# Kernel tuning notes

Hardware: AMD Instinct MI355X
Metric: run time of the kernel (lower is better)

Reference implementation:

```python
import jax, jax.numpy as jnp
import numpy as np

F_DIM = 128; K_RBF = 64; NBLOCKS = 3; NUM_SCC = 1; IBEGIN = 4
N_RES_INT = 2; N_RES_AT = 2; N_RES_OUT = 1
NUM_OUTPUTS = 2001; NOUTS = NUM_OUTPUTS + 4  # +4 charge-equilibration channels when num_scc>0
N_ATOMS = 10000; DEG = 32; N_EDGES = N_ATOMS * DEG; NMOL = 64
CUTOFF = 10.0
LOG2 = 0.6931471805599453


def ssp(x):
    # shifted softplus
    return jax.nn.softplus(x) - LOG2


def _residual(x, W1, b1, W2, b2):
    y = ssp(x) @ W1 + b1
    return x + ssp(y) @ W2 + b2


def _forward(R, M, QaAlpha, QaBeta,
             em_W0, em_b0, em_W1, em_b1, em_W2, em_b2,
             iWrbf, iWi, ibi, iWj, ibj, irW1, irb1, irW2, irb2, iWout, ibout, iu,
             arW1, arb1, arW2, arb2, orW1, orb1, orW2, orb2, oW,
             Z, idx_i, idx_j, mol_idx):
    N = R.shape[0]
    dt = R.dtype
    # --- interatomic distances via neighbor gather ---
    Dvec = R[idx_i] - R[idx_j]                                # [E,3]
    Dij = jnp.sqrt(jax.nn.relu(jnp.sum(Dvec * Dvec, -1)))     # [E]
    # --- PhysNet-style exp-Gaussian RBF expansion with smooth cutoff ---
    mu = jnp.linspace(np.exp(-CUTOFF), 1.0, K_RBF).astype(dt)
    gamma = jnp.asarray((K_RBF / (2.0 * (1.0 - np.exp(-CUTOFF)))) ** 2, dt)
    t = Dij / CUTOFF
    cut = jnp.where(Dij < CUTOFF, 1.0 - 6.0 * t**5 + 15.0 * t**4 - 10.0 * t**3, 0.0)
    rbf = cut[:, None] * jnp.exp(-gamma * (jnp.exp(-Dij)[:, None] - mu) ** 2)  # [E,K]

    seg_mol = lambda v: jax.ops.segment_sum(v, mol_idx, num_segments=NMOL)
    Zf = Z.astype(dt)[:, None]
    QaA, QaB = QaAlpha, QaBeta
    QAlpha_mol = seg_mol(QaA)
    QBeta_mol = seg_mol(QaB)
    outputs = None
    nhloss = jnp.asarray(0.0, dt)
    for j in range(NUM_SCC + 1):
        # elemental-modes embedding: f = [Z, M, QaAlpha, QaBeta] -> F
        f = jnp.concatenate([Zf, M[:, None], QaA[:, None], QaB[:, None]], 1)  # [N,4]
        h = ssp(f @ em_W0 + em_b0)
        h = ssp(h @ em_W1 + em_b1)
        x = h @ em_W2 + em_b2                                 # [N,F]
        outputs = jnp.zeros((N, NOUTS), dt)
        nhloss = jnp.asarray(0.0, dt)
        lastout2 = None
        for i in range(NBLOCKS):
            # --- interaction (message passing: gather -> multiply -> segment_sum) ---
            xa = ssp(x)
            g = rbf @ iWrbf[i]                                # [E,F]
            xi = ssp(xa @ iWi[i] + ibi[i])                    # [N,F]
            xj = ssp(xa @ iWj[i] + ibj[i])                    # [N,F]
            m = xi + jax.ops.segment_sum(g * xj[idx_j], idx_i, num_segments=N)
            for r in range(N_RES_INT):
                m = _residual(m, irW1[i, r], irb1[i, r], irW2[i, r], irb2[i, r])
            m = ssp(m)
            x = iu[i] * x + m @ iWout[i] + ibout[i]           # gated update
            for r in range(N_RES_AT):
                x = _residual(x, arW1[i, r], arb1[i, r], arW2[i, r], arb2[i, r])
            # --- output block ---
            xo = x
            for r in range(N_RES_OUT):
                xo = _residual(xo, orW1[i, r], orb1[i, r], orW2[i, r], orb2[i, r])
            out = ssp(xo) @ oW[i]                             # [N,NOUTS]
            outputs = outputs + out
            if j == NUM_SCC:
                out2 = out[IBEGIN:] ** 2                      # row slice, as in source
                if i > 0:
                    nhloss = nhloss + jnp.mean(out2 / (out2 + lastout2 + 1e-7))
                lastout2 = out2
        # --- NSE charge equilibration (per-molecule segment sums) ---
        QaA_n, faA = outputs[:, 0], outputs[:, 1]
        QaB_n, faB = outputs[:, 2], outputs[:, 3]
        QaA = QaA_n + faA * ((QAlpha_mol - seg_mol(QaA_n)) / seg_mol(faA))[mol_idx]
        QaB = QaB_n + faB * ((QBeta_mol - seg_mol(QaB_n)) / seg_mol(faB))[mol_idx]
    outputs = outputs[:, IBEGIN:]
    outputs = jnp.concatenate([outputs[:, :1], jax.nn.relu(outputs[:, 1:])], 1)
    return outputs, Dij, nhloss


def setup_inputs() -> dict:
    key = jax.random.key(0)
    ks = iter(jax.random.split(key, 64))
    nrm = lambda shp, scale: jax.random.normal(next(ks), shp, jnp.float32) * scale
    F, K, B = F_DIM, K_RBF, NBLOCKS
    s = F ** -0.5
    inp = {}
    inp["R"] = jax.random.uniform(next(ks), (N_ATOMS, 3), jnp.float32, 0.0, 12.0)
    inp["M"] = jax.random.uniform(next(ks), (N_ATOMS,), jnp.float32, 1.0, 32.0)
    inp["QaAlpha"] = nrm((N_ATOMS,), 0.1)
    inp["QaBeta"] = nrm((N_ATOMS,), 0.1)
    # elemental-modes MLP 4 -> F -> F -> F
    inp["em_W0"] = nrm((4, F), 0.5); inp["em_b0"] = nrm((F,), 0.01)
    inp["em_W1"] = nrm((F, F), s);   inp["em_b1"] = nrm((F,), 0.01)
    inp["em_W2"] = nrm((F, F), s);   inp["em_b2"] = nrm((F,), 0.01)
    # interaction blocks (stacked over NBLOCKS)
    inp["iWrbf"] = nrm((B, K, F), K ** -0.5)
    inp["iWi"] = nrm((B, F, F), s); inp["ibi"] = nrm((B, F), 0.01)
    inp["iWj"] = nrm((B, F, F), s); inp["ibj"] = nrm((B, F), 0.01)
    inp["irW1"] = nrm((B, N_RES_INT, F, F), s); inp["irb1"] = nrm((B, N_RES_INT, F), 0.01)
    inp["irW2"] = nrm((B, N_RES_INT, F, F), s); inp["irb2"] = nrm((B, N_RES_INT, F), 0.01)
    inp["iWout"] = nrm((B, F, F), s); inp["ibout"] = nrm((B, F), 0.01)
    inp["iu"] = jnp.ones((B, F), jnp.float32)
    inp["arW1"] = nrm((B, N_RES_AT, F, F), s); inp["arb1"] = nrm((B, N_RES_AT, F), 0.01)
    inp["arW2"] = nrm((B, N_RES_AT, F, F), s); inp["arb2"] = nrm((B, N_RES_AT, F), 0.01)
    inp["orW1"] = nrm((B, N_RES_OUT, F, F), s); inp["orb1"] = nrm((B, N_RES_OUT, F), 0.01)
    inp["orW2"] = nrm((B, N_RES_OUT, F, F), s); inp["orb2"] = nrm((B, N_RES_OUT, F), 0.01)
    inp["oW"] = nrm((B, F, NOUTS), s)
    # integer graph structure
    inp["Z"] = jax.random.randint(next(ks), (N_ATOMS,), 1, 36, jnp.int32)
    idx_i = jnp.repeat(jnp.arange(N_ATOMS, dtype=jnp.int32), DEG)
    rnd = jax.random.randint(next(ks), (N_EDGES,), 1, N_ATOMS, jnp.int32)
    inp["idx_i"] = idx_i
    inp["idx_j"] = (idx_i + rnd) % N_ATOMS  # never self -> Dij > 0
    inp["mol_idx"] = ((jnp.arange(N_ATOMS) * NMOL) // N_ATOMS).astype(jnp.int32)
    return inp


def reference(R, M, QaAlpha, QaBeta,
              em_W0, em_b0, em_W1, em_b1, em_W2, em_b2,
              iWrbf, iWi, ibi, iWj, ibj, irW1, irb1, irW2, irb2, iWout, ibout, iu,
              arW1, arb1, arW2, arb2, orW1, orb1, orW2, orb2, oW,
              Z, idx_i, idx_j, mol_idx):
    return _forward(R, M, QaAlpha, QaBeta,
                    em_W0, em_b0, em_W1, em_b1, em_W2, em_b2,
                    iWrbf, iWi, ibi, iWj, ibj, irW1, irb1, irW2, irb2, iWout, ibout, iu,
                    arW1, arb1, arW2, arb2, orW1, orb1, orW2, orb2, oW,
                    Z, idx_i, idx_j, mol_idx)
```

## Files before the change

### kernel.cpp

```cpp
#include <hip/hip_runtime.h>
#include <math.h>

#define NA 10000
#define NAP 10048
#define FD 128
#define KR 64
#define DEGC 32
#define NE (NA*DEGC)
#define NOUTS_C 2005
#define NOUT_FINAL 2001

typedef __attribute__((ext_vector_type(8))) short bh8;
typedef __attribute__((ext_vector_type(4))) float fx4;

__device__ __forceinline__ float sspf(float x){
    float ex = __expf(-fabsf(x));
    return fmaxf(x, 0.0f) + __logf(1.0f + ex) - 0.6931471805599453f;
}
__device__ __forceinline__ unsigned short f2bf(float x){
    unsigned int u = __float_as_uint(x);
    unsigned int r = (u + 0x7fffu + ((u >> 16) & 1u)) >> 16;
    return (unsigned short)r;
}
__device__ __forceinline__ float bf2f(unsigned short u){
    return __uint_as_float(((unsigned int)u) << 16);
}
__device__ __forceinline__ fx4 mfma16(bh8 a, bh8 b, fx4 c){
    return __builtin_amdgcn_mfma_f32_16x16x32_bf16(a, b, c, 0, 0, 0);
}
__device__ __forceinline__ void gll16(const void* g, void* l){
    __builtin_amdgcn_global_load_lds(
        (const __attribute__((address_space(1))) unsigned int*)g,
        (__attribute__((address_space(3))) unsigned int*)l, 16, 0, 0);
}

__global__ void k_dij(const float* __restrict__ R, const int* __restrict__ idx_i,
                      const int* __restrict__ idx_j, float* __restrict__ dij_out){
    int e = blockIdx.x*256 + threadIdx.x;
    if (e >= NE) return;
    int i = idx_i[e], j = idx_j[e];
    float dx = R[i*3+0] - R[j*3+0];
    float dy = R[i*3+1] - R[j*3+1];
    float dz = R[i*3+2] - R[j*3+2];
    dij_out[e] = sqrtf(fmaxf(dx*dx + dy*dy + dz*dz, 0.0f));
}

__global__ void k_init(const float* __restrict__ QaAin, const float* __restrict__ QaBin,
                       const int* __restrict__ mol, float* __restrict__ QaA,
                       float* __restrict__ QaB, float* __restrict__ QAmol,
                       float* __restrict__ QBmol){
    int a = blockIdx.x*256 + threadIdx.x;
    if (a >= NA) return;
    float qa = QaAin[a], qb = QaBin[a];
    QaA[a] = qa; QaB[a] = qb;
    int m = mol[a];
    atomicAdd(&QAmol[m], qa);
    atomicAdd(&QBmol[m], qb);
}

__global__ void k_cvtW(const float* __restrict__ em_W1, const float* __restrict__ em_W2,
                       const float* __restrict__ iWi, const float* __restrict__ iWj,
                       const float* __restrict__ iWout, const float* __restrict__ irW1,
                       const float* __restrict__ irW2, const float* __restrict__ arW1,
                       const float* __restrict__ arW2, const float* __restrict__ orW1,
                       const float* __restrict__ orW2, short* __restrict__ img){
    int gid = blockIdx.x*256 + threadIdx.x;
    if (gid >= 41*2048) return;
    int m = gid >> 11;
    int f = gid & 2047;
    int l15 = f & 15, t = f >> 4;
    int g = t & 3, u = t >> 2;
    int kk = u & 3, cg = u >> 2;
    const float* src; int mm;
    if      (m < 1){ src = em_W1; mm = m; }
    else if (m < 2){ src = em_W2; mm = m-1; }
    else if (m < 5){ src = iWi;   mm = m-2; }
    else if (m < 8){ src = iWj;   mm = m-5; }
    else if (m < 11){ src = iWout; mm = m-8; }
    else if (m < 17){ src = irW1;  mm = m-11; }
    else if (m < 23){ src = irW2;  mm = m-17; }
    else if (m < 29){ src = arW1;  mm = m-23; }
    else if (m < 35){ src = arW2;  mm = m-29; }
    else if (m < 38){ src = orW1;  mm = m-35; }
    else            { src = orW2;  mm = m-38; }
    src += (size_t)mm * 16384;
    int n = cg*16 + l15;
    int k0 = (kk*4 + g)*8;
    bh8 pk;
    #pragma unroll
    for (int j = 0; j < 8; ++j) pk[j] = (short)f2bf(src[(k0+j)*128 + n]);
    *(bh8*)&img[m*16384 + f*8] = pk;
}

__global__ void k_cvtB(const float* __restrict__ em_b1, const float* __restrict__ em_b2,
                       const float* __restrict__ ibi, const float* __restrict__ ibj,
                       const float* __restrict__ ibout, const float* __restrict__ irb1,
                       const float* __restrict__ irb2, const float* __restrict__ arb1,
                       const float* __restrict__ arb2, const float* __restrict__ orb1,
                       const float* __restrict__ orb2, const float* __restrict__ iu,
                       float* __restrict__ bimg){
    int gid = blockIdx.x*256 + threadIdx.x;
    if (gid >= 44*128) return;
    int m = gid >> 7, c = gid & 127;
    float v;
    if      (m < 1)  v = em_b1[c];
    else if (m < 2)  v = em_b2[c];
    else if (m < 5)  v = ibi[(m-2)*128+c];
    else if (m < 8)  v = ibj[(m-5)*128+c];
    else if (m < 11) v = ibout[(m-8)*128+c];
    else if (m < 17) v = irb1[(m-11)*128+c];
    else if (m < 23) v = irb2[(m-17)*128+c];
    else if (m < 29) v = arb1[(m-23)*128+c];
    else if (m < 35) v = arb2[(m-29)*128+c];
    else if (m < 38) v = orb1[(m-35)*128+c];
    else if (m < 41) v = orb2[(m-38)*128+c];
    else             v = iu[(m-41)*128+c];
    bimg[gid] = v;
}

__global__ void k_cvt_wrbf(const float* __restrict__ iWrbf, short* __restrict__ img){
    int gid = blockIdx.x*256 + threadIdx.x;
    if (gid >= 3*1024) return;
    int i = gid >> 10;
    int loc = gid & 1023;
    int n = loc >> 3, s = loc & 7;
    const float* src = iWrbf + (size_t)i*8192;
    int kbase = (s ^ (n&7)) * 8;
    bh8 pk;
    #pragma unroll
    for (int j = 0; j < 8; ++j) pk[j] = (short)f2bf(src[(kbase+j)*128 + n]);
    *(bh8*)&img[i*8192 + n*64 + s*8] = pk;
}

__global__ void k_cvt_oW(const float* __restrict__ oW, short* __restrict__ img){
    int gid = blockIdx.x*256 + threadIdx.x;
    if (gid >= 98304) return;
    int l15 = gid & 15;
    int g = (gid >> 4) & 3;
    int nt = (gid >> 6) & 7;
    int rest = gid >> 9;
    int kk2 = rest % 12, cg = rest / 12;
    int seg = kk2 >> 2;
    int n = cg*128 + nt*16 + l15;
    int kbase = (kk2 & 3)*32 + g*8;
    bh8 pk;
    #pragma unroll
    for (int j = 0; j < 8; ++j){
        float v = (n < NOUTS_C) ? oW[((size_t)seg*128 + kbase + j)*NOUTS_C + n] : 0.0f;
        pk[j] = (short)f2bf(v);
    }
    *(bh8*)&img[(size_t)gid*8] = pk;
}

__device__ __forceinline__ void loadB8(const short* __restrict__ W, int g, int l15, int wv, bh8 b[8]){
    const bh8* Wf = (const bh8*)W;
    const int cgA = wv*2, cgB = wv*2 + 1;
    #pragma unroll
    for (int kk = 0; kk < 4; ++kk){
        b[kk]   = Wf[((cgA*4+kk)*4+g)*16 + l15];
        b[4+kk] = Wf[((cgB*4+kk)*4+g)*16 + l15];
    }
}
__device__ __forceinline__ void gemmB(const short* As, const bh8 b[8], int g, int l15, fx4 acc[2]){
    #pragma unroll
    for (int kk = 0; kk < 4; ++kk){
        int q = kk*4 + g;
        bh8 a = *(const bh8*)&As[l15*128 + ((q ^ (l15&7))*8)];
        acc[0] = mfma16(a, b[kk],   acc[0]);
        acc[1] = mfma16(a, b[4+kk], acc[1]);
    }
}
#define ZACC2 { acc[0]=(fx4){0,0,0,0}; acc[1]=(fx4){0,0,0,0}; }

__device__ __forceinline__ void epiS_ts(short* dst, fx4 acc[2], const float* b,
                                        int g, int c0, int c1){
    float b0 = b[c0], b1 = b[c1];
    #pragma unroll
    for (int r = 0; r < 4; ++r){
        int row = g*4 + r;
        dst[row*128 + (((c0>>3) ^ (row&7))*8) + (c0&7)] = (short)f2bf(sspf(acc[0][r] + b0));
        dst[row*128 + (((c1>>3) ^ (row&7))*8) + (c1&7)] = (short)f2bf(sspf(acc[1][r] + b1));
    }
}
__device__ __forceinline__ void epiS_xadd(float xr[2][4], fx4 acc[2], const float* b,
                                          int c0, int c1){
    float b0 = b[c0], b1 = b[c1];
    #pragma unroll
    for (int r = 0; r < 4; ++r){
        xr[0][r] += acc[0][r] + b0;
        xr[1][r] += acc[1][r] + b1;
    }
}
__device__ __forceinline__ void writeS_xr(short* dst, float xr[2][4], int g, int c0, int c1){
    #pragma unroll
    for (int r = 0; r < 4; ++r){
        int row = g*4 + r;
        dst[row*128 + (((c0>>3) ^ (row&7))*8) + (c0&7)] = (short)f2bf(sspf(xr[0][r]));
        dst[row*128 + (((c1>>3) ^ (row&7))*8) + (c1&7)] = (short)f2bf(sspf(xr[1][r]));
    }
}
__device__ __forceinline__ void storeS_xr(float* dst, float xr[2][4], int r0, int g, int c0, int c1){
    #pragma unroll
    for (int r = 0; r < 4; ++r){
        int row = r0 + g*4 + r;
        dst[(size_t)row*FD + c0] = xr[0][r];
        dst[(size_t)row*FD + c1] = xr[1][r];
    }
}
__device__ __forceinline__ void storeS_ssp(float* dst, fx4 acc[2], const float* b,
                                           int r0, int g, int c0, int c1){
    float b0 = b[c0], b1 = b[c1];
    #pragma unroll
    for (int r = 0; r < 4; ++r){
        int row = r0 + g*4 + r;
        dst[(size_t)row*FD + c0] = sspf(acc[0][r] + b0);
        dst[(size_t)row*FD + c1] = sspf(acc[1][r] + b1);
    }
}
__device__ __forceinline__ void stage_A16(short* As, const float* src, int r0, int tid){
    int row = tid >> 4, cb = tid & 15;
    const float* p = src + (size_t)(r0+row)*FD + cb*8;
    float4 u = *(const float4*)p, v = *(const float4*)(p+4);
    float vv[8] = {u.x,u.y,u.z,u.w,v.x,v.y,v.z,v.w};
    bh8 pk;
    #pragma unroll
    for (int t = 0; t < 8; ++t) pk[t] = (short)f2bf(sspf(vv[t]));
    *(bh8*)&As[row*128 + ((cb ^ (row&7))*8)] = pk;
}

__global__ __launch_bounds__(256) void k_pre(
    const short* __restrict__ wimg, const float* __restrict__ bimg,
    const int* __restrict__ Z, const float* __restrict__ M,
    const float* __restrict__ QaA, const float* __restrict__ QaB,
    const float* __restrict__ em_W0, const float* __restrict__ em_b0,
    float* __restrict__ x, float* __restrict__ xi, float* __restrict__ xj)
{
    __shared__ __align__(16) short As[2048];
    __shared__ __align__(16) short Ts[2048];
    __shared__ float fs[16][4];
    const int tid = threadIdx.x, wv = tid>>6, ln = tid&63, g = ln>>4, l15 = ln&15;
    const int r0 = blockIdx.x*16;
    const int c0 = wv*32 + l15, c1 = c0 + 16;
    bh8 bU[8], bV[8];
    if (tid < 64){
        int rr = tid>>2, k = tid&3;
        int a = r0 + rr;
        fs[rr][k] = (k==0) ? (float)Z[a] : (k==1) ? M[a] : (k==2) ? QaA[a] : QaB[a];
    }
    __syncthreads();
    {
        int row = tid>>4, cb = tid&15;
        bh8 pk;
        #pragma unroll
        for (int t = 0; t < 8; ++t){
            int c = cb*8 + t;
            float v = sspf(em_b0[c] + fs[row][0]*em_W0[c] + fs[row][1]*em_W0[128+c]
                           + fs[row][2]*em_W0[256+c] + fs[row][3]*em_W0[384+c]);
            pk[t] = (short)f2bf(v);
        }
        *(bh8*)&As[row*128 + ((cb ^ (row&7))*8)] = pk;
    }
    loadB8(wimg + 0*16384, g, l15, wv, bU);
    __syncthreads();
    fx4 acc[2];
    float xr[2][4];
    ZACC2; gemmB(As, bU, g, l15, acc);
    loadB8(wimg + 1*16384, g, l15, wv, bV);
    epiS_ts(Ts, acc, bimg + 0*128, g, c0, c1);
    __syncthreads();
    ZACC2; gemmB(Ts, bV, g, l15, acc);
    loadB8(wimg + 2*16384, g, l15, wv, bU);
    {
        const float* b = bimg + 1*128;
        float b0 = b[c0], b1 = b[c1];
        #pragma unroll
        for (int r = 0; r < 4; ++r){
            xr[0][r] = acc[0][r] + b0;
            xr[1][r] = acc[1][r] + b1;
        }
    }
    storeS_xr(x, xr, r0, g, c0, c1);
    writeS_xr(As, xr, g, c0, c1);
    __syncthreads();
    ZACC2; gemmB(As, bU, g, l15, acc);
    loadB8(wimg + 5*16384, g, l15, wv, bV);
    storeS_ssp(xi, acc, bimg + 2*128, r0, g, c0, c1);
    ZACC2; gemmB(As, bV, g, l15, acc);
    storeS_ssp(xj, acc, bimg + 5*128, r0, g, c0, c1);
}

__global__ __launch_bounds__(256) void k_post(
    const short* __restrict__ wimg, const float* __restrict__ bimg,
    const float* __restrict__ mb, float* __restrict__ x,
    short* __restrict__ Aimg, float* __restrict__ xi, float* __restrict__ xj,
    int i, int dodual)
{
    __shared__ __align__(16) short As[2048];
    __shared__ __align__(16) short Ts[2048];
    const int tid = threadIdx.x, wv = tid>>6, ln = tid&63, g = ln>>4, l15 = ln&15;
    const int r0 = blockIdx.x*16;
    const int c0 = wv*32 + l15, c1 = c0 + 16;
    bh8 bU[8], bV[8];
    float xr[2][4];
    #pragma unroll
    for (int r = 0; r < 4; ++r){
        size_t row = (size_t)(r0 + g*4 + r);
        xr[0][r] = mb[row*FD + c0];
        xr[1][r] = mb[row*FD + c1];
    }
    stage_A16(As, mb, r0, tid);
    loadB8(wimg + (size_t)(11+2*i)*16384, g, l15, wv, bU);
    __syncthreads();
    fx4 acc[2];
    ZACC2; gemmB(As, bU, g, l15, acc);
    loadB8(wimg + (size_t)(17+2*i)*16384, g, l15, wv, bV);
    epiS_ts(Ts, acc, bimg + (11+2*i)*128, g, c0, c1);
    __syncthreads();
    ZACC2; gemmB(Ts, bV, g, l15, acc);
    loadB8(wimg + (size_t)(12+2*i)*16384, g, l15, wv, bU);
    epiS_xadd(xr, acc, bimg + (17+2*i)*128, c0, c1);
    writeS_xr(As, xr, g, c0, c1);
    __syncthreads();
    ZACC2; gemmB(As, bU, g, l15, acc);
    loadB8(wimg + (size_t)(18+2*i)*16384, g, l15, wv, bV);
    epiS_ts(Ts, acc, bimg + (12+2*i)*128, g, c0, c1);
    __syncthreads();
    ZACC2; gemmB(Ts, bV, g, l15, acc);
    loadB8(wimg + (size_t)(8+i)*16384, g, l15, wv, bU);
    epiS_xadd(xr, acc, bimg + (18+2*i)*128, c0, c1);
    writeS_xr(As, xr, g, c0, c1);
    __syncthreads();
    ZACC2; gemmB(As, bU, g, l15, acc);
    loadB8(wimg + (size_t)(23+2*i)*16384, g, l15, wv, bV);
    {
        const float* bb = bimg + (8+i)*128;
        const float* uu = bimg + (41+i)*128;
        float b0 = bb[c0], b1 = bb[c1], u0 = uu[c0], u1 = uu[c1];
        #pragma unroll
        for (int r = 0; r < 4; ++r){
            size_t row = (size_t)(r0 + g*4 + r);
            xr[0][r] = u0*x[row*FD + c0] + acc[0][r] + b0;
            xr[1][r] = u1*x[row*FD + c1] + acc[1][r] + b1;
        }
    }
    writeS_xr(Ts, xr, g, c0, c1);
    __syncthreads();
    ZACC2; gemmB(Ts, bV, g, l15, acc);
    loadB8(wimg + (size_t)(29+2*i)*16384, g, l15, wv, bU);
    epiS_ts(As, acc, bimg + (23+2*i)*128, g, c0, c1);
    __syncthreads();
    ZACC2; gemmB(As, bU, g, l15, acc);
    loadB8(wimg + (size_t)(24+2*i)*16384, g, l15, wv, bV);
    epiS_xadd(xr, acc, bimg + (29+2*i)*128, c0, c1);
    writeS_xr(Ts, xr, g, c0, c1);
    __syncthreads();
    ZACC2; gemmB(Ts, bV, g, l15, acc);
    loadB8(wimg + (size_t)(30+2*i)*16384, g, l15, wv, bU);
    epiS_ts(As, acc, bimg + (24+2*i)*128, g, c0, c1);
    __syncthreads();
    ZACC2; gemmB(As, bU, g, l15, acc);
    loadB8(wimg + (size_t)(dodual ? (3+i) : (35+i))*16384, g, l15, wv, bV);
    epiS_xadd(xr, acc, bimg + (30+2*i)*128, c0, c1);
    storeS_xr(x, xr, r0, g, c0, c1);
    writeS_xr(Ts, xr, g, c0, c1);
    __syncthreads();
    if (dodual){
        ZACC2; gemmB(Ts, bV, g, l15, acc);
        loadB8(wimg + (size_t)(6+i)*16384, g, l15, wv, bU);
        storeS_ssp(xi, acc, bimg + (3+i)*128, r0, g, c0, c1);
        ZACC2; gemmB(Ts, bU, g, l15, acc);
        loadB8(wimg + (size_t)(35+i)*16384, g, l15, wv, bV);
        storeS_ssp(xj, acc, bimg + (6+i)*128, r0, g, c0, c1);
        ZACC2; gemmB(Ts, bV, g, l15, acc);
        loadB8(wimg + (size_t)(38+i)*16384, g, l15, wv, bU);
        epiS_ts(As, acc, bimg + (35+i)*128, g, c0, c1);
    } else {
        ZACC2; gemmB(Ts, bV, g, l15, acc);
        loadB8(wimg + (size_t)(38+i)*16384, g, l15, wv, bU);
        epiS_ts(As, acc, bimg + (35+i)*128, g, c0, c1);
    }
    __syncthreads();
    ZACC2; gemmB(As, bU, g, l15, acc);
    {
        const float* bb = bimg + (38+i)*128;
        float b0 = bb[c0], b1 = bb[c1];
        #pragma unroll
        for (int r = 0; r < 4; ++r){
            int row = r0 + g*4 + r;
            float v0 = xr[0][r] + acc[0][r] + b0;
            float v1 = xr[1][r] + acc[1][r] + b1;
            int k0 = i*128 + c0, k1 = i*128 + c1;
            Aimg[(size_t)row*384 + (((k0>>3) ^ (row&7))*8) + (k0&7)] = (short)f2bf(sspf(v0));
            Aimg[(size_t)row*384 + (((k1>>3) ^ (row&7))*8) + (k1&7)] = (short)f2bf(sspf(v1));
        }
    }
}

__global__ __launch_bounds__(256) void k_agg_mfma(
    const float* __restrict__ dij, const short* __restrict__ wri,
    const int* __restrict__ idxj, const float* __restrict__ xi,
    const float* __restrict__ xj, float* __restrict__ mout,
    float gamma, float mu0, float dmu)
{
    __shared__ short Rb[256*64];
    __shared__ short Wr[128*64];
    __shared__ int Jd[256];
    const int tid = threadIdx.x;
    const int wv = tid >> 6, ln = tid & 63;
    const int e0 = blockIdx.x * 256;
    {
        const char* g2 = (const char*)wri;
        char* l2 = (char*)Wr;
        #pragma unroll
        for (int i = 0; i < 4; ++i){
            int off = wv*4096 + i*1024;
            gll16(g2 + off + ln*16, l2 + off);
        }
        Jd[tid] = idxj[e0 + tid];
    }
    {
        float d = dij[e0 + tid];
        float t = d * 0.1f;
        float cut = 0.0f;
        if (d < 10.0f){
            float t2 = t*t, t3 = t2*t, t4 = t2*t2, t5 = t4*t;
            cut = 1.0f - 6.0f*t5 + 15.0f*t4 - 10.0f*t3;
        }
        float ed = __expf(-d);
        int row = tid;
        #pragma unroll
        for (int s = 0; s < 8; ++s){
            bh8 pk;
            #pragma unroll
            for (int jj = 0; jj < 8; ++jj){
                float u = ed - (mu0 + (float)(s*8+jj)*dmu);
                pk[jj] = (short)f2bf(cut * __expf(-gamma*u*u));
            }
            *(bh8*)&Rb[row*64 + ((s ^ (row&7))*8)] = pk;
        }
    }
    __syncthreads();
    const int g = ln >> 4, l15 = ln & 15;
    bh8 a[4][2];
    #pragma unroll
    for (int mt = 0; mt < 4; ++mt){
        int el = wv*64 + mt*16 + l15;
        #pragma unroll
        for (int kk = 0; kk < 2; ++kk)
            a[mt][kk] = *(const bh8*)&Rb[el*64 + (((kk*4+g) ^ (el&7))*8)];
    }
    float pa[2][8];
    #pragma unroll
    for (int q = 0; q < 8; ++q){ pa[0][q]=0.f; pa[1][q]=0.f; }
    #pragma unroll
    for (int h = 0; h < 2; ++h){
        fx4 acc[4][4];
        #pragma unroll
        for (int mt = 0; mt < 4; ++mt)
            #pragma unroll
            for (int nt = 0; nt < 4; ++nt) acc[mt][nt] = (fx4){0,0,0,0};
        #pragma unroll
        for (int kk = 0; kk < 2; ++kk){
            #pragma unroll
            for (int nt = 0; nt < 4; ++nt){
                int n = h*64 + nt*16 + l15;
                bh8 b = *(const bh8*)&Wr[n*64 + (((kk*4+g) ^ (n&7))*8)];
                #pragma unroll
                for (int mt = 0; mt < 4; ++mt)
                    acc[mt][nt] = mfma16(a[mt][kk], b, acc[mt][nt]);
            }
        }
        #pragma unroll
        for (int mt = 0; mt < 4; ++mt){
            int at = mt >> 1;
            int jv[4];
            #pragma unroll
            for (int r = 0; r < 4; ++r) jv[r] = Jd[wv*64 + mt*16 + g*4 + r];
            #pragma unroll
            for (int nt = 0; nt < 4; ++nt){
                int col = h*64 + nt*16 + l15;
                float s = 0.f;
                #pragma unroll
                for (int r = 0; r < 4; ++r)
                    s += acc[mt][nt][r] * xj[(size_t)jv[r]*FD + col];
                pa[at][h*4+nt] += s;
            }
        }
    }
    #pragma unroll
    for (int at = 0; at < 2; ++at)
        #pragma unroll
        for (int q = 0; q < 8; ++q){
            float v = pa[at][q];
            v += __shfl_xor(v, 16);
            v += __shfl_xor(v, 32);
            pa[at][q] = v;
        }
    if (g == 0){
        #pragma unroll
        for (int at = 0; at < 2; ++at){
            int ga = blockIdx.x*8 + wv*2 + at;
            #pragma unroll
            for (int q = 0; q < 8; ++q){
                int col = (q>>2)*64 + (q&3)*16 + l15;
                mout[(size_t)ga*FD + col] = xi[(size_t)ga*FD + col] + pa[at][q];
            }
        }
    }
}

__global__ void k_out4all(const short* __restrict__ Aimg, const float* __restrict__ oW,
                          float* __restrict__ out4){
    int gid = blockIdx.x*256 + threadIdx.x;
    int a = gid >> 6;
    int lane = threadIdx.x & 63;
    if (a >= NA) return;
    float p0=0.f, p1=0.f, p2=0.f, p3=0.f;
    #pragma unroll
    for (int seg = 0; seg < 3; ++seg){
        const float* oWs = oW + (size_t)seg*FD*NOUTS_C;
        int k0 = seg*128 + lane, k1 = k0 + 64;
        float y0 = bf2f((unsigned short)Aimg[(size_t)a*384 + (((k0>>3) ^ (a&7))*8) + (k0&7)]);
        float y1 = bf2f((unsigned short)Aimg[(size_t)a*384 + (((k1>>3) ^ (a&7))*8) + (k1&7)]);
        const float* w0 = oWs + (size_t)lane*NOUTS_C;
        const float* w1 = oWs + (size_t)(lane+64)*NOUTS_C;
        p0 += y0*w0[0] + y1*w1[0];
        p1 += y0*w0[1] + y1*w1[1];
        p2 += y0*w0[2] + y1*w1[2];
        p3 += y0*w0[3] + y1*w1[3];
    }
    #pragma unroll
    for (int off = 32; off > 0; off >>= 1){
        p0 += __shfl_down(p0, off);
        p1 += __shfl_down(p1, off);
        p2 += __shfl_down(p2, off);
        p3 += __shfl_down(p3, off);
    }
    if (lane == 0){
        out4[a*4+0] = p0; out4[a*4+1] = p1;
        out4[a*4+2] = p2; out4[a*4+3] = p3;
    }
}

__global__ void k_molsum(const float* __restrict__ out4, const int* __restrict__ mol,
                         float* __restrict__ sums){
    int a = blockIdx.x*256 + threadIdx.x;
    if (a >= NA) return;
    int m = mol[a];
    atomicAdd(&sums[m],     out4[a*4+0]);
    atomicAdd(&sums[64+m],  out4[a*4+1]);
    atomicAdd(&sums[128+m], out4[a*4+2]);
    atomicAdd(&sums[192+m], out4[a*4+3]);
}

__global__ void k_qaupd(const float* __restrict__ out4, const int* __restrict__ mol,
                        const float* __restrict__ sums, const float* __restrict__ QAmol,
                        const float* __restrict__ QBmol, float* __restrict__ QaA,
                        float* __restrict__ QaB){
    int a = blockIdx.x*256 + threadIdx.x;
    if (a >= NA) return;
    int m = mol[a];
    float qa_n = out4[a*4+0], fa = out4[a*4+1];
    float qb_n = out4[a*4+2], fb = out4[a*4+3];
    QaA[a] = qa_n + fa * ((QAmol[m] - sums[m])     / sums[64+m]);
    QaB[a] = qb_n + fb * ((QBmol[m] - sums[128+m]) / sums[192+m]);
}

__global__ __launch_bounds__(256) void k_final6(
    const short* __restrict__ Aimg, const short* __restrict__ oWfrag,
    float* __restrict__ outp, float* __restrict__ nh_acc)
{
    __shared__ float Cs[4][16][132];
    const int tid = threadIdx.x, wv = tid>>6, ln = tid&63, g = ln>>4, l15 = ln&15;
    const int r0 = blockIdx.x*64 + wv*16;
    const int cg = blockIdx.y;
    const bh8* Bf = (const bh8*)oWfrag + (size_t)cg*6144;
    fx4 osum[8], p2[8];
    #pragma unroll
    for (int nt = 0; nt < 8; ++nt){ osum[nt]=(fx4){0,0,0,0}; p2[nt]=(fx4){0,0,0,0}; }
    float nh = 0.f;
    #pragma unroll
    for (int seg = 0; seg < 3; ++seg){
        fx4 acc[8];
        #pragma unroll
        for (int nt = 0; nt < 8; ++nt) acc[nt] = (fx4){0,0,0,0};
        #pragma unroll
        for (int kkl = 0; kkl < 4; ++kkl){
            int kk2 = seg*4 + kkl;
            int s = kk2*4 + g;
            bh8 a = *(const bh8*)&Aimg[(size_t)(r0+l15)*384 + ((s ^ (l15&7))*8)];
            #pragma unroll
            for (int nt = 0; nt < 8; ++nt){
                bh8 b = Bf[((kk2*8 + nt)*4 + g)*16 + l15];
                acc[nt] = mfma16(a, b, acc[nt]);
            }
        }
        #pragma unroll
        for (int nt = 0; nt < 8; ++nt)
        #pragma unroll
        for (int r = 0; r < 4; ++r){
            float o = acc[nt][r];
            osum[nt][r] += o;
            if (seg > 0){
                int A = r0 + g*4 + r;
                int col = cg*128 + nt*16 + l15;
                if (A >= 4 && A < NA && col < NOUTS_C){
                    float o2 = o*o;
                    float den = o2 + p2[nt][r] + 1e-7f;
                    float rr;
                    asm("v_rcp_f32 %0, %1" : "=v"(rr) : "v"(den));
                    nh += o2 * rr;
                }
            }
            p2[nt][r] = o*o;
        }
    }
    #pragma unroll
    for (int nt = 0; nt < 8; ++nt)
        #pragma unroll
        for (int r = 0; r < 4; ++r)
            Cs[wv][g*4 + r][nt*16 + l15] = osum[nt][r];
    const int cgbase = cg*128;
    #pragma unroll
    for (int r8 = 0; r8 < 16; ++r8){
        int A = r0 + r8;
        if (A < NA){
            size_t orow = (size_t)A*NOUT_FINAL;
            #pragma unroll
            for (int e = 0; e < 2; ++e){
                int colg = cgbase + e*64 + ln;
                if (colg >= 4 && colg < NOUTS_C){
                    float v = Cs[wv][r8][e*64 + ln];
                    if (colg > 4) v = fmaxf(v, 0.f);
                    outp[orow + (colg - 4)] = v;
                }
            }
        }
    }
    #pragma unroll
    for (int off = 32; off > 0; off >>= 1) nh += __shfl_down(nh, off);
    if (ln == 0) atomicAdd(nh_acc, nh);
}

__global__ void k_finalize(const float* __restrict__ nh_acc, float* __restrict__ nh_out){
    *nh_out = *nh_acc * (1.0f / (float)((NA - 4) * NOUTS_C));
}

extern "C" void kernel_launch(void* const* d_in, const int* in_sizes, int n_in,
                              void* d_out, int out_size, void* d_ws, size_t ws_size,
                              hipStream_t stream)
{
    const float* R       = (const float*)d_in[0];
    const float* M       = (const float*)d_in[1];
    const float* QaAlpha = (const float*)d_in[2];
    const float* QaBeta  = (const float*)d_in[3];
    const float* em_W0   = (const float*)d_in[4];
    const float* em_b0   = (const float*)d_in[5];
    const float* em_W1   = (const float*)d_in[6];
    const float* em_b1   = (const float*)d_in[7];
    const float* em_W2   = (const float*)d_in[8];
    const float* em_b2   = (const float*)d_in[9];
    const float* iWrbf   = (const float*)d_in[10];
    const float* iWi     = (const float*)d_in[11];
    const float* ibi     = (const float*)d_in[12];
    const float* iWj     = (const float*)d_in[13];
    const float* ibj     = (const float*)d_in[14];
    const float* irW1    = (const float*)d_in[15];
    const float* irb1    = (const float*)d_in[16];
    const float* irW2    = (const float*)d_in[17];
    const float* irb2    = (const float*)d_in[18];
    const float* iWout   = (const float*)d_in[19];
    const float* ibout   = (const float*)d_in[20];
    const float* iu      = (const float*)d_in[21];
    const float* arW1    = (const float*)d_in[22];
    const float* arb1    = (const float*)d_in[23];
    const float* arW2    = (const float*)d_in[24];
    const float* arb2    = (const float*)d_in[25];
    const float* orW1    = (const float*)d_in[26];
    const float* orb1    = (const float*)d_in[27];
    const float* orW2    = (const float*)d_in[28];
    const float* orb2    = (const float*)d_in[29];
    const float* oW      = (const float*)d_in[30];
    const int*   Z       = (const int*)d_in[31];
    const int*   idx_i   = (const int*)d_in[32];
    const int*   idx_j   = (const int*)d_in[33];
    const int*   mol     = (const int*)d_in[34];

    float* out    = (float*)d_out;
    float* dij    = out + (size_t)NA*NOUT_FINAL;
    float* nh_out = dij + NE;

    float* fbase = (float*)d_ws;
    size_t fo = 0;
    float* x    = fbase + fo; fo += (size_t)NA*FD;
    float* xi   = fbase + fo; fo += (size_t)NA*FD;
    float* xj   = fbase + fo; fo += (size_t)NA*FD;
    float* mb   = fbase + fo; fo += (size_t)NA*FD;
    float* out4 = fbase + fo; fo += (size_t)NA*4;
    float* sums = fbase + fo; fo += 256;
    float* QAmol= fbase + fo; fo += 64;
    float* QBmol= fbase + fo; fo += 64;
    float* nhac = fbase + fo; fo += 1;
    float* QaA  = fbase + fo; fo += NA;
    float* QaB  = fbase + fo; fo += NA;
    float* bimg = fbase + fo; fo += 44*128;
    size_t sboff = ((fo*4 + 63) / 64) * 64;
    short* sbase = (short*)((char*)d_ws + sboff);
    size_t so = 0;
    short* wimg   = sbase + so; so += (size_t)41*16384;
    short* wrbf   = sbase + so; so += (size_t)3*8192;
    short* oWfrag = sbase + so; so += (size_t)98304*8;
    short* Aimg   = sbase + so; so += (size_t)NAP*384;

    hipMemsetAsync(sums, 0, (size_t)(256 + 64 + 64 + 1)*sizeof(float), stream);
    hipMemsetAsync(Aimg + (size_t)NA*384, 0, (size_t)(NAP-NA)*384*sizeof(short), stream);

    k_cvtW<<<(41*2048+255)/256, 256, 0, stream>>>(em_W1, em_W2, iWi, iWj, iWout,
                                                  irW1, irW2, arW1, arW2, orW1, orW2, wimg);
    k_cvtB<<<(44*128+255)/256, 256, 0, stream>>>(em_b1, em_b2, ibi, ibj, ibout,
                                                 irb1, irb2, arb1, arb2, orb1, orb2, iu, bimg);
    k_cvt_wrbf<<<(3*1024+255)/256, 256, 0, stream>>>(iWrbf, wrbf);
    k_cvt_oW<<<(98304+255)/256, 256, 0, stream>>>(oW, oWfrag);

    k_dij<<<(NE+255)/256, 256, 0, stream>>>(R, idx_i, idx_j, dij);
    k_init<<<(NA+255)/256, 256, 0, stream>>>(QaAlpha, QaBeta, mol, QaA, QaB, QAmol, QBmol);

    double expn = exp(-10.0);
    float gamma = (float)pow(64.0/(2.0*(1.0-expn)), 2.0);
    float mu0 = (float)expn;
    float dmu = (float)((1.0-expn)/63.0);

    for (int j = 0; j <= 1; ++j){
        k_pre<<<625, 256, 0, stream>>>(wimg, bimg, Z, M, QaA, QaB, em_W0, em_b0, x, xi, xj);
        for (int i = 0; i < 3; ++i){
            k_agg_mfma<<<1250, 256, 0, stream>>>(dij, wrbf + (size_t)i*8192, idx_j, xi, xj, mb,
                                                 gamma, mu0, dmu);
            k_post<<<625, 256, 0, stream>>>(wimg, bimg, mb, x, Aimg, xi, xj, i, (i<2) ? 1 : 0);
        }
        if (j == 0){
            k_out4all<<<(NA*64)/256, 256, 0, stream>>>(Aimg, oW, out4);
            k_molsum<<<(NA+255)/256, 256, 0, stream>>>(out4, mol, sums);
            k_qaupd<<<(NA+255)/256, 256, 0, stream>>>(out4, mol, sums, QAmol, QBmol, QaA, QaB);
        }
    }
    k_final6<<<dim3(157,16), 256, 0, stream>>>(Aimg, oWfrag, out, nhac);
    k_finalize<<<1, 1, 0, stream>>>(nhac, nh_out);
}
```

Baseline: 991.6 us.

## Keep A fragments in registers and double-buffer B across four column groups

The final output GEMM kernel now loads each wave's 12 A fragments into registers once and reuses them across four 128-column groups per block, cutting the grid from 16 to 4 column blocks. B fragments are software-pipelined with two register buffers (bU/bV), so the next k-slice, or the next column group's first slice, is prefetched while MFMAs run on the current one. This removes repeated A reloads and hides B load latency, at the cost of more registers, lower occupancy, and fewer blocks (628 instead of 2512).

```diff
diff --git a/kernel.cpp b/kernel.cpp
--- a/kernel.cpp
+++ b/kernel.cpp
@@ -566,73 +566,103 @@
     QaB[a] = qb_n + fb * ((QBmol[m] - sums[128+m]) / sums[192+m]);
 }
 
-__global__ __launch_bounds__(256) void k_final6(
+__global__ __launch_bounds__(256) void k_final7(
     const short* __restrict__ Aimg, const short* __restrict__ oWfrag,
     float* __restrict__ outp, float* __restrict__ nh_acc)
 {
     __shared__ float Cs[4][16][132];
     const int tid = threadIdx.x, wv = tid>>6, ln = tid&63, g = ln>>4, l15 = ln&15;
     const int r0 = blockIdx.x*64 + wv*16;
-    const int cg = blockIdx.y;
-    const bh8* Bf = (const bh8*)oWfrag + (size_t)cg*6144;
-    fx4 osum[8], p2[8];
-    #pragma unroll
-    for (int nt = 0; nt < 8; ++nt){ osum[nt]=(fx4){0,0,0,0}; p2[nt]=(fx4){0,0,0,0}; }
+    const int arow = r0 + l15;
+    bh8 af[12];
+    #pragma unroll
+    for (int kk2 = 0; kk2 < 12; ++kk2){
+        int s = kk2*4 + g;
+        af[kk2] = *(const bh8*)&Aimg[(size_t)arow*384 + ((s ^ (l15&7))*8)];
+    }
     float nh = 0.f;
-    #pragma unroll
-    for (int seg = 0; seg < 3; ++seg){
-        fx4 acc[8];
-        #pragma unroll
-        for (int nt = 0; nt < 8; ++nt) acc[nt] = (fx4){0,0,0,0};
-        #pragma unroll
-        for (int kkl = 0; kkl < 4; ++kkl){
-            int kk2 = seg*4 + kkl;
-            int s = kk2*4 + g;
-            bh8 a = *(const bh8*)&Aimg[(size_t)(r0+l15)*384 + ((s ^ (l15&7))*8)];
-            #pragma unroll
-            for (int nt = 0; nt < 8; ++nt){
-                bh8 b = Bf[((kk2*8 + nt)*4 + g)*16 + l15];
-                acc[nt] = mfma16(a, b, acc[nt]);
-            }
-        }
-        #pragma unroll
-        for (int nt = 0; nt < 8; ++nt)
-        #pragma unroll
-        for (int r = 0; r < 4; ++r){
-            float o = acc[nt][r];
-            osum[nt][r] += o;
-            if (seg > 0){
-                int A = r0 + g*4 + r;
-                int col = cg*128 + nt*16 + l15;
-                if (A >= 4 && A < NA && col < NOUTS_C){
-                    float o2 = o*o;
-                    float den = o2 + p2[nt][r] + 1e-7f;
-                    float rr;
-                    asm("v_rcp_f32 %0, %1" : "=v"(rr) : "v"(den));
-                    nh += o2 * rr;
+    const int cg0 = blockIdx.y*4;
+    const bh8* Bf = (const bh8*)oWfrag + (size_t)cg0*6144;
+    bh8 bU[8], bV[8];
+    #pragma unroll
+    for (int nt = 0; nt < 8; ++nt) bU[nt] = Bf[(nt*4 + g)*16 + l15];
+    #pragma unroll
+    for (int cgl = 0; cgl < 4; ++cgl){
+        const int cg = cg0 + cgl;
+        const bh8* Bc = (const bh8*)oWfrag + (size_t)cg*6144;
+        const bh8* Bn = Bc + 6144;
+        fx4 osum[8], p2[8];
+        #pragma unroll
+        for (int nt = 0; nt < 8; ++nt){ osum[nt]=(fx4){0,0,0,0}; p2[nt]=(fx4){0,0,0,0}; }
+        #pragma unroll
+        for (int seg = 0; seg < 3; ++seg){
+            fx4 acc[8];
+            #pragma unroll
+            for (int nt = 0; nt < 8; ++nt) acc[nt] = (fx4){0,0,0,0};
+            #pragma unroll
+            for (int kkl = 0; kkl < 4; ++kkl){
+                const int kk2 = seg*4 + kkl;
+                if ((kk2 & 1) == 0){
+                    #pragma unroll
+                    for (int nt = 0; nt < 8; ++nt)
+                        bV[nt] = Bc[(((kk2+1)*8 + nt)*4 + g)*16 + l15];
+                    #pragma unroll
+                    for (int nt = 0; nt < 8; ++nt)
+                        acc[nt] = mfma16(af[kk2], bU[nt], acc[nt]);
+                } else {
+                    if (kk2 < 11){
+                        #pragma unroll
+                        for (int nt = 0; nt < 8; ++nt)
+                            bU[nt] = Bc[(((kk2+1)*8 + nt)*4 + g)*16 + l15];
+                    } else if (cgl < 3){
+                        #pragma unroll
+                        for (int nt = 0; nt < 8; ++nt)
+                            bU[nt] = Bn[(nt*4 + g)*16 + l15];
+                    }
+                    #pragma unroll
+                    for (int nt = 0; nt < 8; ++nt)
+                        acc[nt] = mfma16(af[kk2], bV[nt], acc[nt]);
                 }
             }
-            p2[nt][r] = o*o;
-        }
-    }
-    #pragma unroll
-    for (int nt = 0; nt < 8; ++nt)
-        #pragma unroll
-        for (int r = 0; r < 4; ++r)
-            Cs[wv][g*4 + r][nt*16 + l15] = osum[nt][r];
-    const int cgbase = cg*128;
-    #pragma unroll
-    for (int r8 = 0; r8 < 16; ++r8){
-        int A = r0 + r8;
-        if (A < NA){
-            size_t orow = (size_t)A*NOUT_FINAL;
-            #pragma unroll
-            for (int e = 0; e < 2; ++e){
-                int colg = cgbase + e*64 + ln;
-                if (colg >= 4 && colg < NOUTS_C){
-                    float v = Cs[wv][r8][e*64 + ln];
-                    if (colg > 4) v = fmaxf(v, 0.f);
-                    outp[orow + (colg - 4)] = v;
+            #pragma unroll
+            for (int nt = 0; nt < 8; ++nt)
+            #pragma unroll
+            for (int r = 0; r < 4; ++r){
+                float o = acc[nt][r];
+                osum[nt][r] += o;
+                if (seg > 0){
+                    int A = r0 + g*4 + r;
+                    int col = cg*128 + nt*16 + l15;
+                    if (A >= 4 && A < NA && col < NOUTS_C){
+                        float o2 = o*o;
+                        float den = o2 + p2[nt][r] + 1e-7f;
+                        float rr;
+                        asm("v_rcp_f32 %0, %1" : "=v"(rr) : "v"(den));
+                        nh += o2 * rr;
+                    }
+                }
+                p2[nt][r] = o*o;
+            }
+        }
+        #pragma unroll
+        for (int nt = 0; nt < 8; ++nt)
+            #pragma unroll
+            for (int r = 0; r < 4; ++r)
+                Cs[wv][g*4 + r][nt*16 + l15] = osum[nt][r];
+        const int cgbase = cg*128;
+        #pragma unroll
+        for (int r8 = 0; r8 < 16; ++r8){
+            int A = r0 + r8;
+            if (A < NA){
+                size_t orow = (size_t)A*NOUT_FINAL;
+                #pragma unroll
+                for (int e = 0; e < 2; ++e){
+                    int colg = cgbase + e*64 + ln;
+                    if (colg >= 4 && colg < NOUTS_C){
+                        float v = Cs[wv][r8][e*64 + ln];
+                        if (colg > 4) v = fmaxf(v, 0.f);
+                        outp[orow + (colg - 4)] = v;
+                    }
                 }
             }
         }
@@ -743,6 +773,6 @@
             k_qaupd<<<(NA+255)/256, 256, 0, stream>>>(out4, mol, sums, QAmol, QBmol, QaA, QaB);
         }
     }
-    k_final6<<<dim3(157,16), 256, 0, stream>>>(Aimg, oWfrag, out, nhac);
+    k_final7<<<dim3(157,4), 256, 0, stream>>>(Aimg, oWfrag, out, nhac);
     k_finalize<<<1, 1, 0, stream>>>(nhac, nh_out);
 }
```

Measured after the change: 974.8 us. Within noise of the previous version (-1.7%).
